# Performance work log

Measured on AMD Instinct MI355X. Metric: run time of the kernel, lower is better.

## Reference

```python
import jax, jax.numpy as jnp
import numpy as np

B, N, M, IN, OUT, H = 256, 2048, 64, 128, 64, 100
EPS = 1e-8


def setup_inputs() -> dict:
    key = jax.random.key(0)
    ks = jax.random.split(key, 32)
    rn = lambda i, shp, sc=1.0: jax.random.normal(ks[i], shp, jnp.float32) * sc
    d = {}
    d["x"] = rn(0, (B, IN))
    d["Wc"] = rn(1, (IN, H), 1.0 / np.sqrt(IN)); d["bc"] = jnp.zeros((H,), jnp.float32)
    d["Wo"] = rn(2, (M, OUT), 1.0 / np.sqrt(M)); d["bo"] = jnp.zeros((OUT,), jnp.float32)
    i = 3
    for p in ("r", "w"):
        d[p + "_W_beta"] = rn(i, (H, 1), 0.1); i += 1; d[p + "_b_beta"] = jnp.zeros((1,), jnp.float32)
        d[p + "_W_gamma"] = rn(i, (H, 1), 0.1); i += 1; d[p + "_b_gamma"] = jnp.zeros((1,), jnp.float32)
        d[p + "_W_g"] = rn(i, (H, 1), 0.1); i += 1; d[p + "_b_g"] = jnp.zeros((1,), jnp.float32)
        # tiny shift weights + positive bias keep the shifted weighting positive
        # (the original code takes tilde_w ** gamma, which NaNs for negative base)
        d[p + "_W_s"] = rn(i, (H, 3), 0.001); i += 1; d[p + "_b_s"] = jnp.full((3,), 0.5, jnp.float32)
        d[p + "_W_k"] = rn(i, (H, M), 0.1); i += 1; d[p + "_b_k"] = jnp.zeros((M,), jnp.float32)
    d["w_W_e"] = rn(i, (H, M), 0.1); i += 1; d["w_b_e"] = jnp.zeros((M,), jnp.float32)
    d["w_W_a"] = rn(i, (H, M), 0.1); i += 1; d["w_b_a"] = jnp.zeros((M,), jnp.float32)
    d["r_attn_bias"] = rn(i, (B, N)); i += 1
    d["w_attn_bias"] = rn(i, (B, N)); i += 1
    d["memory_bias"] = rn(i, (B, N, M))
    return d


def _addressing(mem, attn, k, beta, g, s, gamma):
    # cosine similarity of key k [B,M] against each memory row [B,N,M]
    kn = jnp.maximum(jnp.linalg.norm(k, axis=1, keepdims=True), EPS)        # [B,1]
    mn = jnp.maximum(jnp.linalg.norm(mem, axis=2), EPS)                     # [B,N]
    cos = jnp.einsum('bm,bnm->bn', k, mem) / (kn * mn)                      # [B,N]
    w_c = jax.nn.softmax(beta * cos, axis=-1)                               # beta [B,1]
    w_g = g * w_c + (1.0 - g) * attn                                        # interpolation
    # circular 3-tap convolution: tw[i] = s0*w[i-1] + s1*w[i] + s2*w[i+1]
    tw = (s[:, 0:1] * jnp.roll(w_g, 1, axis=1)
          + s[:, 1:2] * w_g
          + s[:, 2:3] * jnp.roll(w_g, -1, axis=1))
    p = tw ** gamma                                                         # sharpening
    return p / (EPS + p.sum(axis=1, keepdims=True))


def _forward(x, Wc, bc, Wo, bo,
             r_W_beta, r_b_beta, r_W_gamma, r_b_gamma, r_W_g, r_b_g,
             r_W_s, r_b_s, r_W_k, r_b_k,
             w_W_beta, w_b_beta, w_W_gamma, w_b_gamma, w_W_g, w_b_g,
             w_W_s, w_b_s, w_W_k, w_b_k,
             w_W_e, w_b_e, w_W_a, w_b_a,
             r_attn_bias, w_attn_bias, memory_bias):
    h = x @ Wc + bc                                                         # controller [B,100]

    # ---- send: write-head addressing + erase/add write ----
    beta_w = jax.nn.softplus(h @ w_W_beta + w_b_beta)
    gamma_w = 1.0 + jax.nn.softplus(h @ w_W_gamma + w_b_gamma)
    g_w = jax.nn.sigmoid(h @ w_W_g + w_b_g)
    s_w = h @ w_W_s + w_b_s
    k_w = h @ w_W_k + w_b_k
    w_attn0 = jax.nn.softmax(w_attn_bias, axis=1)
    w_attn = _addressing(memory_bias, w_attn0, k_w, beta_w, g_w, s_w, gamma_w)
    e = jax.nn.sigmoid(h @ w_W_e + w_b_e)                                   # [B,M]
    a = h @ w_W_a + w_b_a                                                   # [B,M]
    mem = (memory_bias * (1.0 - w_attn[:, :, None] * e[:, None, :])
           + w_attn[:, :, None] * a[:, None, :])                            # [B,N,M]

    # ---- receive: read-head addressing + read + output ----
    beta_r = jax.nn.softplus(h @ r_W_beta + r_b_beta)
    gamma_r = 1.0 + jax.nn.softplus(h @ r_W_gamma + r_b_gamma)
    g_r = jax.nn.sigmoid(h @ r_W_g + r_b_g)
    s_r = h @ r_W_s + r_b_s
    k_r = h @ r_W_k + r_b_k
    r_attn0 = jax.nn.softmax(r_attn_bias, axis=1)
    r_attn = _addressing(mem, r_attn0, k_r, beta_r, g_r, s_r, gamma_r)
    r = jnp.einsum('bn,bnm->bm', r_attn, mem)                               # read vector [B,M]
    out = jax.nn.sigmoid(r @ Wo + bo)                                       # [B,OUT]
    return out


def reference(x, Wc, bc, Wo, bo,
              r_W_beta, r_b_beta, r_W_gamma, r_b_gamma, r_W_g, r_b_g,
              r_W_s, r_b_s, r_W_k, r_b_k,
              w_W_beta, w_b_beta, w_W_gamma, w_b_gamma, w_W_g, w_b_g,
              w_W_s, w_b_s, w_W_k, w_b_k,
              w_W_e, w_b_e, w_W_a, w_b_a,
              r_attn_bias, w_attn_bias, memory_bias):
    return _forward(x, Wc, bc, Wo, bo,
                    r_W_beta, r_b_beta, r_W_gamma, r_b_gamma, r_W_g, r_b_g,
                    r_W_s, r_b_s, r_W_k, r_b_k,
                    w_W_beta, w_b_beta, w_W_gamma, w_b_gamma, w_W_g, w_b_g,
                    w_W_s, w_b_s, w_W_k, w_b_k,
                    w_W_e, w_b_e, w_W_a, w_b_a,
                    r_attn_bias, w_attn_bias, memory_bias)
```

## Files before the change

### kernel.cpp

```cpp
#include <hip/hip_runtime.h>
#include <hip/hip_bf16.h>
#include <math.h>

#define BB 256
#define NN 2048
#define MM 64
#define INF_ 128
#define HH 100
#define EPSF 1e-8f
#define PITCH (NN + 1)

struct Ptrs { const float* p[32]; };

__device__ __forceinline__ float softplusf(float x) {
    return fmaxf(x, 0.0f) + log1pf(__expf(-fabsf(x)));
}
__device__ __forceinline__ float sigmoidf(float x) {
    return 1.0f / (1.0f + __expf(-x));
}
__device__ __forceinline__ float fpowf(float x, float g) {
    return __expf(g * __logf(x));
}

__device__ __forceinline__ void bredN(float& a, float& b, bool ismax, float* red)
{
    #pragma unroll
    for (int m = 32; m; m >>= 1) {
        float ta = __shfl_xor(a, m), tb = __shfl_xor(b, m);
        if (ismax) { a = fmaxf(a, ta); b = fmaxf(b, tb); }
        else       { a += ta; b += tb; }
    }
    const int wid = threadIdx.x >> 6;
    if ((threadIdx.x & 63) == 0) { red[wid] = a; red[16 + wid] = b; }
    __syncthreads();
    float ra = red[0], rb = red[16];
    #pragma unroll
    for (int w = 1; w < 16; ++w) {
        if (ismax) { ra = fmaxf(ra, red[w]); rb = fmaxf(rb, red[16 + w]); }
        else       { ra += red[w]; rb += red[16 + w]; }
    }
    __syncthreads();
    a = ra; b = rb;
}

__global__ void __launch_bounds__(1024, 8) k_fused(Ptrs in,
                                                   const float* __restrict__ mb,
                                                   float* __restrict__ out)
{
    __shared__ float xs[INF_];
    __shared__ float hs[HH];
    __shared__ float pk_w[MM], pk_r[MM], pe[MM], pa[MM];
    __shared__ float psc[20];
    __shared__ float summ6[6 * PITCH];
    __shared__ float ats[NN];
    __shared__ float watt[NN];
    __shared__ float ratt[NN];
    __shared__ float red[32];
    __shared__ float rv[64];

    const int b = blockIdx.x, tid = threadIdx.x;
    const int lane = tid & 63, wv = tid >> 6;
    const int grp = tid >> 3, l8 = tid & 7;

    if (tid < INF_) xs[tid] = in.p[0][b * INF_ + tid];
    __syncthreads();

    if (tid < HH) {
        const float* Wc = in.p[1];
        float acc = in.p[2][tid];
        #pragma unroll 8
        for (int i = 0; i < INF_; ++i)
            acc = fmaf(xs[i], Wc[i * HH + tid], acc);
        hs[tid] = acc;
    }
    __syncthreads();

    if (wv < 4) {
        const int m = lane;
        const float* W; const float* bi;
        if      (wv == 0) { W = in.p[23]; bi = in.p[24]; }
        else if (wv == 1) { W = in.p[13]; bi = in.p[14]; }
        else if (wv == 2) { W = in.p[25]; bi = in.p[26]; }
        else              { W = in.p[27]; bi = in.p[28]; }
        float acc = bi[m];
        #pragma unroll 10
        for (int j = 0; j < HH; ++j)
            acc = fmaf(hs[j], W[j * 64 + m], acc);
        if      (wv == 0) pk_w[m] = acc;
        else if (wv == 1) pk_r[m] = acc;
        else if (wv == 2) pe[m]   = sigmoidf(acc);
        else              pa[m]   = acc;
    } else {
        const int s = wv - 4;
        const float* W; float bia; int strd = 1, c = 0;
        if      (s == 0) { W = in.p[15]; bia = in.p[16][0]; }
        else if (s == 1) { W = in.p[17]; bia = in.p[18][0]; }
        else if (s == 2) { W = in.p[19]; bia = in.p[20][0]; }
        else if (s == 3) { W = in.p[5];  bia = in.p[6][0]; }
        else if (s == 4) { W = in.p[7];  bia = in.p[8][0]; }
        else if (s == 5) { W = in.p[9];  bia = in.p[10][0]; }
        else if (s < 9)  { W = in.p[21]; c = s - 6; bia = in.p[22][c]; strd = 3; }
        else             { W = in.p[11]; c = s - 9; bia = in.p[12][c]; strd = 3; }
        float v = 0.f;
        if (lane < HH)      v = hs[lane] * W[lane * strd + c];
        if (lane < HH - 64) v = fmaf(hs[lane + 64], W[(lane + 64) * strd + c], v);
        #pragma unroll
        for (int m2 = 32; m2; m2 >>= 1) v += __shfl_xor(v, m2);
        if (lane == 0) {
            float r = v + bia;
            if      (s == 0) psc[15] = softplusf(r);
            else if (s == 1) psc[2]  = 1.0f + softplusf(r);
            else if (s == 2) psc[4]  = sigmoidf(r);
            else if (s == 3) psc[16] = softplusf(r);
            else if (s == 4) psc[3]  = 1.0f + softplusf(r);
            else if (s == 5) psc[5]  = sigmoidf(r);
            else if (s < 9)  psc[6 + c] = r;
            else             psc[9 + c] = r;
        }
    }
    __syncthreads();

    if (wv == 0) {
        float v = pk_w[lane] * pk_w[lane];
        #pragma unroll
        for (int m2 = 32; m2; m2 >>= 1) v += __shfl_xor(v, m2);
        if (lane == 0) psc[0] = psc[15] / fmaxf(sqrtf(v), EPSF);
    }
    if (wv == 1) {
        float v = pk_r[lane] * pk_r[lane];
        #pragma unroll
        for (int m2 = 32; m2; m2 >>= 1) v += __shfl_xor(v, m2);
        if (lane == 0) psc[1] = psc[16] / fmaxf(sqrtf(v), EPSF);
    }
    if (wv == 2) {
        float v = pk_r[lane] * pa[lane];
        #pragma unroll
        for (int m2 = 32; m2; m2 >>= 1) v += __shfl_xor(v, m2);
        if (lane == 0) psc[12] = v;
    }
    if (wv == 3) {
        float v = pa[lane] * pa[lane];
        #pragma unroll
        for (int m2 = 32; m2; m2 >>= 1) v += __shfl_xor(v, m2);
        if (lane == 0) psc[13] = v;
    }
    __syncthreads();

    {
        float kw[8], kr[8], ev[8], av[8];
        #pragma unroll
        for (int j = 0; j < 8; ++j) {
            kw[j] = pk_w[l8 * 8 + j];
            kr[j] = pk_r[l8 * 8 + j];
            ev[j] = pe[l8 * 8 + j];
            av[j] = pa[l8 * 8 + j];
        }
        const float kra_ = psc[12], saa_ = psc[13];
        const float4* base = reinterpret_cast<const float4*>(mb + (size_t)b * NN * MM);

        #pragma unroll 4
        for (int it = 0; it < 16; ++it) {
            const int n = it * 128 + grp;
            float4 v0 = base[n * 16 + 2 * l8];
            float4 v1 = base[n * 16 + 2 * l8 + 1];
            float f[8] = {v0.x, v0.y, v0.z, v0.w, v1.x, v1.y, v1.z, v1.w};

            float acc[8];
            #pragma unroll
            for (int j = 0; j < 8; ++j) acc[j] = 0.f;
            #pragma unroll
            for (int j = 0; j < 8; ++j) {
                const float m = f[j];
                const float em = ev[j] * m;
                acc[0] = fmaf(kw[j], m, acc[0]);
                acc[1] = fmaf(m, m, acc[1]);
                acc[2] = fmaf(kr[j], m, acc[2]);
                acc[3] = fmaf(kr[j], em, acc[3]);
                acc[4] = fmaf(m, av[j] - em, acc[4]);
                acc[5] = fmaf(em, fmaf(-2.f, av[j], em), acc[5]);
            }

            float k1[4];
            #pragma unroll
            for (int k = 0; k < 4; ++k) {
                float snd = (l8 & 1) ? acc[2 * k] : acc[2 * k + 1];
                float rcv = __shfl_xor(snd, 1);
                k1[k] = ((l8 & 1) ? acc[2 * k + 1] : acc[2 * k]) + rcv;
            }
            float k2[2];
            #pragma unroll
            for (int k = 0; k < 2; ++k) {
                float snd = (l8 & 2) ? k1[2 * k] : k1[2 * k + 1];
                float rcv = __shfl_xor(snd, 2);
                k2[k] = ((l8 & 2) ? k1[2 * k + 1] : k1[2 * k]) + rcv;
            }
            float snd = (l8 & 4) ? k2[0] : k2[1];
            float rcv = __shfl_xor(snd, 4);
            float tot = ((l8 & 4) ? k2[1] : k2[0]) + rcv;

            if (l8 == 3) tot = kra_ - tot;
            if (l8 == 5) tot += saa_;
            if (l8 < 6) summ6[l8 * PITCH + n] = tot;
        }
    }
    __syncthreads();

    {
        const float g = psc[4], gamma = psc[2];
        const float s0c = psc[6], s1c = psc[7], s2c = psc[8];
        const float coef = psc[0];

        float lgr[2], bbr[2];
        float mL = -1e30f, mB = -1e30f;
        #pragma unroll
        for (int k = 0; k < 2; ++k) {
            int i = tid + k * 1024;
            float lw = summ6[i];
            float s0 = summ6[PITCH + i];
            float lg = coef * lw / fmaxf(sqrtf(s0), EPSF);
            lgr[k] = lg; mL = fmaxf(mL, lg);
            float bb = in.p[30][(size_t)b * NN + i]; bbr[k] = bb; mB = fmaxf(mB, bb);
        }
        bredN(mL, mB, true, red);

        float pw[2], pb[2];
        float sL = 0.f, sB = 0.f;
        #pragma unroll
        for (int k = 0; k < 2; ++k) {
            pw[k] = __expf(lgr[k] - mL);
            pb[k] = __expf(bbr[k] - mB);
            sL += pw[k]; sB += pb[k];
        }
        bredN(sL, sB, false, red);
        const float iL = 1.0f / sL, iB = 1.0f / sB;

        #pragma unroll
        for (int k = 0; k < 2; ++k) {
            int i = tid + k * 1024;
            ats[i] = g * pw[k] * iL + (1.0f - g) * pb[k] * iB;
        }
        __syncthreads();

        float pv[2]; float ps = 0.f;
        #pragma unroll
        for (int k = 0; k < 2; ++k) {
            int i = tid + k * 1024;
            float tw = s0c * ats[(i + NN - 1) & (NN - 1)]
                     + s1c * ats[i]
                     + s2c * ats[(i + 1) & (NN - 1)];
            float p = fpowf(tw, gamma);
            pv[k] = p; ps += p;
        }
        float dmy = 0.f;
        bredN(ps, dmy, false, red);
        const float inv = 1.0f / (EPSF + ps);
        #pragma unroll
        for (int k = 0; k < 2; ++k) {
            int i = tid + k * 1024;
            watt[i] = pv[k] * inv;
        }
        __syncthreads();
    }

    {
        const float g = psc[5], gamma = psc[3];
        const float s0c = psc[9], s1c = psc[10], s2c = psc[11];
        const float coef = psc[1];

        float lgr[2], bbr[2];
        float mL = -1e30f, mB = -1e30f;
        #pragma unroll
        for (int k = 0; k < 2; ++k) {
            int i = tid + k * 1024;
            const float w  = watt[i];
            const float s0 = summ6[PITCH + i];
            const float d1 = summ6[2 * PITCH + i];
            const float v1 = summ6[3 * PITCH + i];
            const float u1 = summ6[4 * PITCH + i];
            const float u2 = summ6[5 * PITCH + i];
            const float dot = fmaf(w, v1, d1);
            float nrm2 = s0 + 2.f * w * u1 + w * w * u2;
            nrm2 = fmaxf(nrm2, 0.f);
            float lg = coef * dot / fmaxf(sqrtf(nrm2), EPSF);
            lgr[k] = lg; mL = fmaxf(mL, lg);
            float bb = in.p[29][(size_t)b * NN + i]; bbr[k] = bb; mB = fmaxf(mB, bb);
        }
        bredN(mL, mB, true, red);

        float pw[2], pb[2];
        float sL = 0.f, sB = 0.f;
        #pragma unroll
        for (int k = 0; k < 2; ++k) {
            pw[k] = __expf(lgr[k] - mL);
            pb[k] = __expf(bbr[k] - mB);
            sL += pw[k]; sB += pb[k];
        }
        bredN(sL, sB, false, red);
        const float iL = 1.0f / sL, iB = 1.0f / sB;

        #pragma unroll
        for (int k = 0; k < 2; ++k) {
            int i = tid + k * 1024;
            ats[i] = g * pw[k] * iL + (1.0f - g) * pb[k] * iB;
        }
        __syncthreads();

        float pv[2]; float ps = 0.f;
        #pragma unroll
        for (int k = 0; k < 2; ++k) {
            int i = tid + k * 1024;
            float tw = s0c * ats[(i + NN - 1) & (NN - 1)]
                     + s1c * ats[i]
                     + s2c * ats[(i + 1) & (NN - 1)];
            float p = fpowf(tw, gamma);
            pv[k] = p; ps += p;
        }
        float dmy = 0.f;
        bredN(ps, dmy, false, red);
        const float inv = 1.0f / (EPSF + ps);
        #pragma unroll
        for (int k = 0; k < 2; ++k) {
            int i = tid + k * 1024;
            ratt[i] = pv[k] * inv;
        }
        __syncthreads();
    }

    float* wp1 = summ6;
    float* wp2 = summ6 + 1024;

    float tval = ratt[tid] * watt[tid] + ratt[tid + 1024] * watt[tid + 1024];
    {
        float dmy = 0.f;
        bredN(tval, dmy, false, red);
    }

    {
        float a1[8], a2[8];
        #pragma unroll
        for (int j = 0; j < 8; ++j) { a1[j] = 0.f; a2[j] = 0.f; }
        const float4* base = reinterpret_cast<const float4*>(mb + (size_t)b * NN * MM);

        #pragma unroll 4
        for (int it = 0; it < 16; ++it) {
            const int n = it * 128 + grp;
            const float c1 = ratt[n];
            const float c2 = c1 * watt[n];
            float4 v0 = base[n * 16 + 2 * l8];
            float4 v1 = base[n * 16 + 2 * l8 + 1];
            float f[8] = {v0.x, v0.y, v0.z, v0.w, v1.x, v1.y, v1.z, v1.w};
            #pragma unroll
            for (int j = 0; j < 8; ++j) {
                a1[j] = fmaf(c1, f[j], a1[j]);
                a2[j] = fmaf(c2, f[j], a2[j]);
            }
        }
        #pragma unroll
        for (int j = 0; j < 8; ++j) {
            #pragma unroll
            for (int mask = 8; mask < 64; mask <<= 1) {
                a1[j] += __shfl_xor(a1[j], mask);
                a2[j] += __shfl_xor(a2[j], mask);
            }
        }
        if (lane < 8) {
            #pragma unroll
            for (int j = 0; j < 8; ++j) {
                wp1[wv * 64 + lane * 8 + j] = a1[j];
                wp2[wv * 64 + lane * 8 + j] = a2[j];
            }
        }
    }
    __syncthreads();

    if (tid < 64) {
        float S1 = 0.f, S2 = 0.f;
        #pragma unroll
        for (int w8 = 0; w8 < 16; ++w8) {
            S1 += wp1[w8 * 64 + tid];
            S2 += wp2[w8 * 64 + tid];
        }
        rv[tid] = S1 - pe[tid] * S2 + tval * pa[tid];
    }
    __syncthreads();

    if (tid < 64) {
        const float* Wo = in.p[3];
        float o = in.p[4][tid];
        #pragma unroll 4
        for (int m = 0; m < 64; ++m) o = fmaf(rv[m], Wo[m * 64 + tid], o);
        out[(size_t)b * 64 + tid] = sigmoidf(o);
    }
}

extern "C" void kernel_launch(void* const* d_in, const int* in_sizes, int n_in,
                              void* d_out, int out_size, void* d_ws, size_t ws_size,
                              hipStream_t stream)
{
    Ptrs in;
    for (int i = 0; i < 32; ++i) in.p[i] = (const float*)d_in[i];
    const float* mb = (const float*)d_in[31];

    k_fused<<<BB, 1024, 0, stream>>>(in, mb, (float*)d_out);
}
```

Before: 65.19 us.

## Prefetch memory tiles into registers to overlap loads with softmax phases

The first pass over memory now batches eight rows of float4 loads into registers before computing, which raises memory-level parallelism. The first half of the memory tile for the second pass, plus the read-head attention bias, is prefetched into registers before the write and read addressing phases, so those global loads overlap with the softmax reductions. The second half is loaded at the start of the read pass. The shared-memory pitch changes to 2056, and the launch bound drops its min-blocks hint, which trades occupancy for the extra registers the prefetch needs.

```diff
diff --git a/kernel.cpp b/kernel.cpp
--- a/kernel.cpp
+++ b/kernel.cpp
@@ -8,7 +8,7 @@
 #define INF_ 128
 #define HH 100
 #define EPSF 1e-8f
-#define PITCH (NN + 1)
+#define PITCH 2056
 
 struct Ptrs { const float* p[32]; };
 
@@ -43,9 +43,9 @@
     a = ra; b = rb;
 }
 
-__global__ void __launch_bounds__(1024, 8) k_fused(Ptrs in,
-                                                   const float* __restrict__ mb,
-                                                   float* __restrict__ out)
+__global__ void __launch_bounds__(1024) k_fused(Ptrs in,
+                                                const float* __restrict__ mb,
+                                                float* __restrict__ out)
 {
     __shared__ float xs[INF_];
     __shared__ float hs[HH];
@@ -146,6 +146,8 @@
     }
     __syncthreads();
 
+    const float4* base = reinterpret_cast<const float4*>(mb + (size_t)b * NN * MM);
+
     {
         float kw[8], kr[8], ev[8], av[8];
         #pragma unroll
@@ -156,54 +158,71 @@
             av[j] = pa[l8 * 8 + j];
         }
         const float kra_ = psc[12], saa_ = psc[13];
-        const float4* base = reinterpret_cast<const float4*>(mb + (size_t)b * NN * MM);
-
-        #pragma unroll 4
-        for (int it = 0; it < 16; ++it) {
-            const int n = it * 128 + grp;
-            float4 v0 = base[n * 16 + 2 * l8];
-            float4 v1 = base[n * 16 + 2 * l8 + 1];
-            float f[8] = {v0.x, v0.y, v0.z, v0.w, v1.x, v1.y, v1.z, v1.w};
-
-            float acc[8];
-            #pragma unroll
-            for (int j = 0; j < 8; ++j) acc[j] = 0.f;
-            #pragma unroll
-            for (int j = 0; j < 8; ++j) {
-                const float m = f[j];
-                const float em = ev[j] * m;
-                acc[0] = fmaf(kw[j], m, acc[0]);
-                acc[1] = fmaf(m, m, acc[1]);
-                acc[2] = fmaf(kr[j], m, acc[2]);
-                acc[3] = fmaf(kr[j], em, acc[3]);
-                acc[4] = fmaf(m, av[j] - em, acc[4]);
-                acc[5] = fmaf(em, fmaf(-2.f, av[j], em), acc[5]);
-            }
-
-            float k1[4];
-            #pragma unroll
-            for (int k = 0; k < 4; ++k) {
-                float snd = (l8 & 1) ? acc[2 * k] : acc[2 * k + 1];
-                float rcv = __shfl_xor(snd, 1);
-                k1[k] = ((l8 & 1) ? acc[2 * k + 1] : acc[2 * k]) + rcv;
-            }
-            float k2[2];
-            #pragma unroll
-            for (int k = 0; k < 2; ++k) {
-                float snd = (l8 & 2) ? k1[2 * k] : k1[2 * k + 1];
-                float rcv = __shfl_xor(snd, 2);
-                k2[k] = ((l8 & 2) ? k1[2 * k + 1] : k1[2 * k]) + rcv;
-            }
-            float snd = (l8 & 4) ? k2[0] : k2[1];
-            float rcv = __shfl_xor(snd, 4);
-            float tot = ((l8 & 4) ? k2[1] : k2[0]) + rcv;
-
-            if (l8 == 3) tot = kra_ - tot;
-            if (l8 == 5) tot += saa_;
-            if (l8 < 6) summ6[l8 * PITCH + n] = tot;
-        }
-    }
-    __syncthreads();
+
+        #pragma unroll
+        for (int half = 0; half < 2; ++half) {
+            float4 vA[8], vB[8];
+            #pragma unroll
+            for (int it = 0; it < 8; ++it) {
+                const int n = (half * 8 + it) * 128 + grp;
+                vA[it] = base[n * 16 + 2 * l8];
+                vB[it] = base[n * 16 + 2 * l8 + 1];
+            }
+            #pragma unroll
+            for (int it = 0; it < 8; ++it) {
+                const int n = (half * 8 + it) * 128 + grp;
+                float f[8] = {vA[it].x, vA[it].y, vA[it].z, vA[it].w,
+                              vB[it].x, vB[it].y, vB[it].z, vB[it].w};
+                float acc[8];
+                #pragma unroll
+                for (int j = 0; j < 8; ++j) acc[j] = 0.f;
+                #pragma unroll
+                for (int j = 0; j < 8; ++j) {
+                    const float m = f[j];
+                    const float em = ev[j] * m;
+                    acc[0] = fmaf(kw[j], m, acc[0]);
+                    acc[1] = fmaf(m, m, acc[1]);
+                    acc[2] = fmaf(kr[j], m, acc[2]);
+                    acc[3] = fmaf(kr[j], em, acc[3]);
+                    acc[4] = fmaf(m, av[j] - em, acc[4]);
+                    acc[5] = fmaf(em, fmaf(-2.f, av[j], em), acc[5]);
+                }
+                float k1[4];
+                #pragma unroll
+                for (int k = 0; k < 4; ++k) {
+                    float snd = (l8 & 1) ? acc[2 * k] : acc[2 * k + 1];
+                    float rcv = __shfl_xor(snd, 1);
+                    k1[k] = ((l8 & 1) ? acc[2 * k + 1] : acc[2 * k]) + rcv;
+                }
+                float k2[2];
+                #pragma unroll
+                for (int k = 0; k < 2; ++k) {
+                    float snd = (l8 & 2) ? k1[2 * k] : k1[2 * k + 1];
+                    float rcv = __shfl_xor(snd, 2);
+                    k2[k] = ((l8 & 2) ? k1[2 * k + 1] : k1[2 * k]) + rcv;
+                }
+                float snd = (l8 & 4) ? k2[0] : k2[1];
+                float rcv = __shfl_xor(snd, 4);
+                float tot = ((l8 & 4) ? k2[1] : k2[0]) + rcv;
+
+                if (l8 == 3) tot = kra_ - tot;
+                if (l8 == 5) tot += saa_;
+                if (l8 < 6) summ6[l8 * PITCH + n] = tot;
+            }
+        }
+    }
+    __syncthreads();
+
+    float4 dA[8], dB[8];
+    #pragma unroll
+    for (int it = 0; it < 8; ++it) {
+        const int n = it * 128 + grp;
+        dA[it] = base[n * 16 + 2 * l8];
+        dB[it] = base[n * 16 + 2 * l8 + 1];
+    }
+    float rbb[2];
+    rbb[0] = in.p[29][(size_t)b * NN + tid];
+    rbb[1] = in.p[29][(size_t)b * NN + tid + 1024];
 
     {
         const float g = psc[4], gamma = psc[2];
@@ -267,7 +286,7 @@
         const float s0c = psc[9], s1c = psc[10], s2c = psc[11];
         const float coef = psc[1];
 
-        float lgr[2], bbr[2];
+        float lgr[2];
         float mL = -1e30f, mB = -1e30f;
         #pragma unroll
         for (int k = 0; k < 2; ++k) {
@@ -283,7 +302,7 @@
             nrm2 = fmaxf(nrm2, 0.f);
             float lg = coef * dot / fmaxf(sqrtf(nrm2), EPSF);
             lgr[k] = lg; mL = fmaxf(mL, lg);
-            float bb = in.p[29][(size_t)b * NN + i]; bbr[k] = bb; mB = fmaxf(mB, bb);
+            mB = fmaxf(mB, rbb[k]);
         }
         bredN(mL, mB, true, red);
 
@@ -292,7 +311,7 @@
         #pragma unroll
         for (int k = 0; k < 2; ++k) {
             pw[k] = __expf(lgr[k] - mL);
-            pb[k] = __expf(bbr[k] - mB);
+            pb[k] = __expf(rbb[k] - mB);
             sL += pw[k]; sB += pb[k];
         }
         bredN(sL, sB, false, red);
@@ -339,22 +358,42 @@
         float a1[8], a2[8];
         #pragma unroll
         for (int j = 0; j < 8; ++j) { a1[j] = 0.f; a2[j] = 0.f; }
-        const float4* base = reinterpret_cast<const float4*>(mb + (size_t)b * NN * MM);
-
-        #pragma unroll 4
-        for (int it = 0; it < 16; ++it) {
+
+        float4 eA[8], eB[8];
+        #pragma unroll
+        for (int it = 0; it < 8; ++it) {
+            const int n = (8 + it) * 128 + grp;
+            eA[it] = base[n * 16 + 2 * l8];
+            eB[it] = base[n * 16 + 2 * l8 + 1];
+        }
+
+        #pragma unroll
+        for (int it = 0; it < 8; ++it) {
             const int n = it * 128 + grp;
             const float c1 = ratt[n];
             const float c2 = c1 * watt[n];
-            float4 v0 = base[n * 16 + 2 * l8];
-            float4 v1 = base[n * 16 + 2 * l8 + 1];
-            float f[8] = {v0.x, v0.y, v0.z, v0.w, v1.x, v1.y, v1.z, v1.w};
+            float f[8] = {dA[it].x, dA[it].y, dA[it].z, dA[it].w,
+                          dB[it].x, dB[it].y, dB[it].z, dB[it].w};
             #pragma unroll
             for (int j = 0; j < 8; ++j) {
                 a1[j] = fmaf(c1, f[j], a1[j]);
                 a2[j] = fmaf(c2, f[j], a2[j]);
             }
         }
+        #pragma unroll
+        for (int it = 0; it < 8; ++it) {
+            const int n = (8 + it) * 128 + grp;
+            const float c1 = ratt[n];
+            const float c2 = c1 * watt[n];
+            float f[8] = {eA[it].x, eA[it].y, eA[it].z, eA[it].w,
+                          eB[it].x, eB[it].y, eB[it].z, eB[it].w};
+            #pragma unroll
+            for (int j = 0; j < 8; ++j) {
+                a1[j] = fmaf(c1, f[j], a1[j]);
+                a2[j] = fmaf(c2, f[j], a2[j]);
+            }
+        }
+
         #pragma unroll
         for (int j = 0; j < 8; ++j) {
             #pragma unroll
```

Measured after the change: 80.30 us. 23.2% more time.

## Remap memory streaming to 16 lanes per row with software-prefetched float4 loads

Applied to the files above, without the earlier changes.

Both passes over the per-batch memory tensor now assign 16 threads per row (one float4 each) instead of 8 threads with two float4 each, and use a 4-deep register prefetch pipeline so each load is issued four iterations ahead of its use. The reduction tree gains an extra xor-8 shuffle to combine the two 8-lane halves, and the final read reduction is adjusted accordingly. PITCH is changed from N+1 to a padded 2056, and the occupancy hint in launch bounds is dropped. The goal is to hide global-memory latency and make loads fully coalesced, at the cost of more shuffles per row and higher register pressure.

```diff
diff --git a/kernel.cpp b/kernel.cpp
--- a/kernel.cpp
+++ b/kernel.cpp
@@ -8,7 +8,7 @@
 #define INF_ 128
 #define HH 100
 #define EPSF 1e-8f
-#define PITCH (NN + 1)
+#define PITCH 2056
 
 struct Ptrs { const float* p[32]; };
 
@@ -43,9 +43,61 @@
     a = ra; b = rb;
 }
 
-__global__ void __launch_bounds__(1024, 8) k_fused(Ptrs in,
-                                                   const float* __restrict__ mb,
-                                                   float* __restrict__ out)
+#define PROC_B(V_, IT_)                                                     \
+    {                                                                       \
+        const int n = (IT_) * 64 + g16;                                     \
+        float f[4] = {V_.x, V_.y, V_.z, V_.w};                              \
+        float acc[8];                                                       \
+        _Pragma("unroll")                                                   \
+        for (int j = 0; j < 8; ++j) acc[j] = 0.f;                           \
+        _Pragma("unroll")                                                   \
+        for (int j = 0; j < 4; ++j) {                                       \
+            const float m = f[j];                                           \
+            const float em = ev[j] * m;                                     \
+            acc[0] = fmaf(kw[j], m, acc[0]);                                \
+            acc[1] = fmaf(m, m, acc[1]);                                    \
+            acc[2] = fmaf(kr[j], m, acc[2]);                                \
+            acc[3] = fmaf(kr[j], em, acc[3]);                               \
+            acc[4] = fmaf(m, av[j] - em, acc[4]);                           \
+            acc[5] = fmaf(em, fmaf(-2.f, av[j], em), acc[5]);               \
+        }                                                                   \
+        float k1[4];                                                        \
+        _Pragma("unroll")                                                   \
+        for (int k = 0; k < 4; ++k) {                                       \
+            float snd = (l8 & 1) ? acc[2 * k] : acc[2 * k + 1];             \
+            float rcv = __shfl_xor(snd, 1);                                 \
+            k1[k] = ((l8 & 1) ? acc[2 * k + 1] : acc[2 * k]) + rcv;         \
+        }                                                                   \
+        float k2[2];                                                        \
+        _Pragma("unroll")                                                   \
+        for (int k = 0; k < 2; ++k) {                                       \
+            float snd = (l8 & 2) ? k1[2 * k] : k1[2 * k + 1];               \
+            float rcv = __shfl_xor(snd, 2);                                 \
+            k2[k] = ((l8 & 2) ? k1[2 * k + 1] : k1[2 * k]) + rcv;           \
+        }                                                                   \
+        float snd = (l8 & 4) ? k2[0] : k2[1];                               \
+        float rcv = __shfl_xor(snd, 4);                                     \
+        float tot = ((l8 & 4) ? k2[1] : k2[0]) + rcv;                       \
+        tot += __shfl_xor(tot, 8);          \
+        if (l16 == 3) tot = kra_ - tot;                  \
+        if (l16 == 5) tot += saa_;                      \
+        if (l16 < 6) summ6[l16 * PITCH + n] = tot;                          \
+    }
+
+#define PROC_D(V_, IT_)                                                     \
+    {                                                                       \
+        const int n = (IT_) * 64 + g16;                                     \
+        const float c1 = ratt[n];                                           \
+        const float c2 = c1 * watt[n];                                      \
+        a1[0] = fmaf(c1, V_.x, a1[0]);  a2[0] = fmaf(c2, V_.x, a2[0]);      \
+        a1[1] = fmaf(c1, V_.y, a1[1]);  a2[1] = fmaf(c2, V_.y, a2[1]);      \
+        a1[2] = fmaf(c1, V_.z, a1[2]);  a2[2] = fmaf(c2, V_.z, a2[2]);      \
+        a1[3] = fmaf(c1, V_.w, a1[3]);  a2[3] = fmaf(c2, V_.w, a2[3]);      \
+    }
+
+__global__ void __launch_bounds__(1024) k_fused(Ptrs in,
+                                                const float* __restrict__ mb,
+                                                float* __restrict__ out)
 {
     __shared__ float xs[INF_];
     __shared__ float hs[HH];
@@ -60,7 +112,8 @@
 
     const int b = blockIdx.x, tid = threadIdx.x;
     const int lane = tid & 63, wv = tid >> 6;
-    const int grp = tid >> 3, l8 = tid & 7;
+    const int g16 = tid >> 4, l16 = tid & 15;
+    const int l8 = l16 & 7;
 
     if (tid < INF_) xs[tid] = in.p[0][b * INF_ + tid];
     __syncthreads();
@@ -146,62 +199,32 @@
     }
     __syncthreads();
 
+    const float4* base = reinterpret_cast<const float4*>(mb + (size_t)b * NN * MM);
+
     {
-        float kw[8], kr[8], ev[8], av[8];
-        #pragma unroll
-        for (int j = 0; j < 8; ++j) {
-            kw[j] = pk_w[l8 * 8 + j];
-            kr[j] = pk_r[l8 * 8 + j];
-            ev[j] = pe[l8 * 8 + j];
-            av[j] = pa[l8 * 8 + j];
+        float kw[4], kr[4], ev[4], av[4];
+        #pragma unroll
+        for (int j = 0; j < 4; ++j) {
+            kw[j] = pk_w[l16 * 4 + j];
+            kr[j] = pk_r[l16 * 4 + j];
+            ev[j] = pe[l16 * 4 + j];
+            av[j] = pa[l16 * 4 + j];
         }
         const float kra_ = psc[12], saa_ = psc[13];
-        const float4* base = reinterpret_cast<const float4*>(mb + (size_t)b * NN * MM);
-
-        #pragma unroll 4
-        for (int it = 0; it < 16; ++it) {
-            const int n = it * 128 + grp;
-            float4 v0 = base[n * 16 + 2 * l8];
-            float4 v1 = base[n * 16 + 2 * l8 + 1];
-            float f[8] = {v0.x, v0.y, v0.z, v0.w, v1.x, v1.y, v1.z, v1.w};
-
-            float acc[8];
-            #pragma unroll
-            for (int j = 0; j < 8; ++j) acc[j] = 0.f;
-            #pragma unroll
-            for (int j = 0; j < 8; ++j) {
-                const float m = f[j];
-                const float em = ev[j] * m;
-                acc[0] = fmaf(kw[j], m, acc[0]);
-                acc[1] = fmaf(m, m, acc[1]);
-                acc[2] = fmaf(kr[j], m, acc[2]);
-                acc[3] = fmaf(kr[j], em, acc[3]);
-                acc[4] = fmaf(m, av[j] - em, acc[4]);
-                acc[5] = fmaf(em, fmaf(-2.f, av[j], em), acc[5]);
-            }
-
-            float k1[4];
-            #pragma unroll
-            for (int k = 0; k < 4; ++k) {
-                float snd = (l8 & 1) ? acc[2 * k] : acc[2 * k + 1];
-                float rcv = __shfl_xor(snd, 1);
-                k1[k] = ((l8 & 1) ? acc[2 * k + 1] : acc[2 * k]) + rcv;
-            }
-            float k2[2];
-            #pragma unroll
-            for (int k = 0; k < 2; ++k) {
-                float snd = (l8 & 2) ? k1[2 * k] : k1[2 * k + 1];
-                float rcv = __shfl_xor(snd, 2);
-                k2[k] = ((l8 & 2) ? k1[2 * k + 1] : k1[2 * k]) + rcv;
-            }
-            float snd = (l8 & 4) ? k2[0] : k2[1];
-            float rcv = __shfl_xor(snd, 4);
-            float tot = ((l8 & 4) ? k2[1] : k2[0]) + rcv;
-
-            if (l8 == 3) tot = kra_ - tot;
-            if (l8 == 5) tot += saa_;
-            if (l8 < 6) summ6[l8 * PITCH + n] = tot;
-        }
+
+        float4 v0 = base[(0 * 64 + g16) * 16 + l16];
+        float4 v1 = base[(1 * 64 + g16) * 16 + l16];
+        float4 v2 = base[(2 * 64 + g16) * 16 + l16];
+        float4 v3 = base[(3 * 64 + g16) * 16 + l16];
+
+        #pragma unroll 1
+        for (int it = 0; it < 28; it += 4) {
+            PROC_B(v0, it);     v0 = base[((it + 4) * 64 + g16) * 16 + l16];
+            PROC_B(v1, it + 1); v1 = base[((it + 5) * 64 + g16) * 16 + l16];
+            PROC_B(v2, it + 2); v2 = base[((it + 6) * 64 + g16) * 16 + l16];
+            PROC_B(v3, it + 3); v3 = base[((it + 7) * 64 + g16) * 16 + l16];
+        }
+        PROC_B(v0, 28); PROC_B(v1, 29); PROC_B(v2, 30); PROC_B(v3, 31);
     }
     __syncthreads();
 
@@ -336,38 +359,36 @@
     }
 
     {
-        float a1[8], a2[8];
-        #pragma unroll
-        for (int j = 0; j < 8; ++j) { a1[j] = 0.f; a2[j] = 0.f; }
-        const float4* base = reinterpret_cast<const float4*>(mb + (size_t)b * NN * MM);
-
-        #pragma unroll 4
-        for (int it = 0; it < 16; ++it) {
-            const int n = it * 128 + grp;
-            const float c1 = ratt[n];
-            const float c2 = c1 * watt[n];
-            float4 v0 = base[n * 16 + 2 * l8];
-            float4 v1 = base[n * 16 + 2 * l8 + 1];
-            float f[8] = {v0.x, v0.y, v0.z, v0.w, v1.x, v1.y, v1.z, v1.w};
+        float a1[4], a2[4];
+        #pragma unroll
+        for (int j = 0; j < 4; ++j) { a1[j] = 0.f; a2[j] = 0.f; }
+
+        float4 v0 = base[(0 * 64 + g16) * 16 + l16];
+        float4 v1 = base[(1 * 64 + g16) * 16 + l16];
+        float4 v2 = base[(2 * 64 + g16) * 16 + l16];
+        float4 v3 = base[(3 * 64 + g16) * 16 + l16];
+
+        #pragma unroll 1
+        for (int it = 0; it < 28; it += 4) {
+            PROC_D(v0, it);     v0 = base[((it + 4) * 64 + g16) * 16 + l16];
+            PROC_D(v1, it + 1); v1 = base[((it + 5) * 64 + g16) * 16 + l16];
+            PROC_D(v2, it + 2); v2 = base[((it + 6) * 64 + g16) * 16 + l16];
+            PROC_D(v3, it + 3); v3 = base[((it + 7) * 64 + g16) * 16 + l16];
+        }
+        PROC_D(v0, 28); PROC_D(v1, 29); PROC_D(v2, 30); PROC_D(v3, 31);
+
+        #pragma unroll
+        for (int j = 0; j < 4; ++j) {
+            a1[j] += __shfl_xor(a1[j], 16);
+            a1[j] += __shfl_xor(a1[j], 32);
+            a2[j] += __shfl_xor(a2[j], 16);
+            a2[j] += __shfl_xor(a2[j], 32);
+        }
+        if (lane < 16) {
             #pragma unroll
-            for (int j = 0; j < 8; ++j) {
-                a1[j] = fmaf(c1, f[j], a1[j]);
-                a2[j] = fmaf(c2, f[j], a2[j]);
-            }
-        }
-        #pragma unroll
-        for (int j = 0; j < 8; ++j) {
-            #pragma unroll
-            for (int mask = 8; mask < 64; mask <<= 1) {
-                a1[j] += __shfl_xor(a1[j], mask);
-                a2[j] += __shfl_xor(a2[j], mask);
-            }
-        }
-        if (lane < 8) {
-            #pragma unroll
-            for (int j = 0; j < 8; ++j) {
-                wp1[wv * 64 + lane * 8 + j] = a1[j];
-                wp2[wv * 64 + lane * 8 + j] = a2[j];
+            for (int j = 0; j < 4; ++j) {
+                wp1[wv * 64 + lane * 4 + j] = a1[j];
+                wp2[wv * 64 + lane * 4 + j] = a2[j];
             }
         }
     }
```

New measurement: 71.19 us. 1.09x slower.
